# Kernel optimization log

Hardware: AMD Instinct MI355X
Metric: run time of the kernel (lower is better)

The kernel has to match this reference:

```python
import jax, jax.numpy as jnp
import numpy as np

H = 256   # hidden_size
IN = 2    # adding-problem input features
B, T = 128, 1024


def setup_inputs() -> dict:
    key = jax.random.key(0)
    ks = jax.random.split(key, 12)
    sc = 1.0 / np.sqrt(H)
    u = lambda k, shape: jax.random.uniform(k, shape, minval=-sc, maxval=sc, dtype=jnp.float32)
    return {
        "x": jax.random.normal(ks[0], (B, T, IN), dtype=jnp.float32),
        # GRU weights (torch layout: [3H, in], gate order r, z, n)
        "W_ih": u(ks[1], (3 * H, IN)),
        "W_hh": u(ks[2], (3 * H, H)),
        "b_ih": u(ks[3], (3 * H,)),
        "b_hh": u(ks[4], (3 * H,)),
        # adaptive momentum coefficient beta_t = sigmoid(x W + h U + b)
        "Wb_x": u(ks[5], (IN, 1)),
        "Wb_h": u(ks[6], (H, 1)),
        "b_beta": jnp.zeros((1,), dtype=jnp.float32),
        # momentum step size s (learnable scalar)
        "s": jnp.ones((), dtype=jnp.float32),
        # read-out head Linear(H, 1)
        "W_head": u(ks[7], (1, H)),
        "b_head": u(ks[8], (1,)),
    }


def reference(x, W_ih, W_hh, b_ih, b_hh, Wb_x, Wb_h, b_beta, s, W_head, b_head):
    Bm = x.shape[0]

    def step(carry, x_t):
        h, v = carry                                    # h: [B,H], v: [B,3H]
        beta = jax.nn.sigmoid(x_t @ Wb_x + h @ Wb_h + b_beta)   # [B,1]
        p = x_t @ W_ih.T + b_ih                         # input projection [B,3H]
        v = beta * v + s * p                            # momentum buffer
        gh = h @ W_hh.T + b_hh                          # hidden projection [B,3H]
        vr, vz, vn = jnp.split(v, 3, axis=-1)
        hr, hz, hn = jnp.split(gh, 3, axis=-1)
        r = jax.nn.sigmoid(vr + hr)
        z = jax.nn.sigmoid(vz + hz)
        n = jnp.tanh(vn + r * hn)
        h_new = (1.0 - z) * n + z * h
        return (h_new, v), beta[:, 0]

    h0 = jnp.zeros((Bm, H), dtype=x.dtype)
    v0 = jnp.zeros((Bm, 3 * H), dtype=x.dtype)
    (hT, _), betas = jax.lax.scan(step, (h0, v0), jnp.transpose(x, (1, 0, 2)))
    out = hT @ W_head.T + b_head                        # head on last timestep, [B,1]
    return (out, betas.T)                               # betas: [B,T]
```

## Files before the change

### kernel.cpp

```cpp
#include <hip/hip_runtime.h>

#define HID 256
#define TLEN 1024
#define BATCH 128

typedef _Float16 half2_t __attribute__((ext_vector_type(2)));

__device__ __forceinline__ float fexp2(float x) { return __builtin_amdgcn_exp2f(x); }
__device__ __forceinline__ float frcp(float x)  { return __builtin_amdgcn_rcpf(x); }
__device__ __forceinline__ float fast_sigmoid(float x) {
  return frcp(1.0f + fexp2(-1.442695040888963f * x));
}
__device__ __forceinline__ float fast_tanh(float x) {
  float e = fexp2(2.885390081777927f * x);
  return 1.0f - 2.0f * frcp(e + 1.0f);
}
__device__ __forceinline__ float dot2acc(half2_t a, half2_t b, float c) {
  return __builtin_amdgcn_fdot2(a, b, c, false);
}

#if defined(__has_builtin) && __has_builtin(__builtin_amdgcn_sdot4)
#define SDOT4(a, b, c) __builtin_amdgcn_sdot4((int)(a), (int)(b), (c), false)
#else
__device__ __forceinline__ int SDOT4(int a, int b, int c) {
#pragma unroll
  for (int e = 0; e < 4; ++e)
    c += ((a << (24 - 8 * e)) >> 24) * ((b << (24 - 8 * e)) >> 24);
  return c;
}
#endif

#define DPP_ADD_F(var, ctrl, rmask)                                            \
  var += __builtin_bit_cast(float, __builtin_amdgcn_update_dpp(                \
      0, __builtin_bit_cast(int, var), (ctrl), (rmask), 0xf, true))
#define DPP_PAIR_SUM_I(var)                                                    \
  var += __builtin_amdgcn_update_dpp(0, (var), 0xB1, 0xf, 0xf, true)
#define DPP_MOV_I(dst, src, ctrl)                                              \
  dst = __builtin_amdgcn_update_dpp(0, (src), (ctrl), 0xf, 0xf, true)

__device__ __forceinline__ float wave_sum63(float p) {
  DPP_ADD_F(p, 0x111, 0xf);
  DPP_ADD_F(p, 0x112, 0xf);
  DPP_ADD_F(p, 0x114, 0xf);
  DPP_ADD_F(p, 0x118, 0xf);
  DPP_ADD_F(p, 0x142, 0xa);
  DPP_ADD_F(p, 0x143, 0xc);
  return p;
}

#define LDS_BARRIER() asm volatile("s_waitcnt lgkmcnt(0)\n\ts_barrier" ::: "memory")

__global__ void quant_whh(const float* __restrict__ W_hh, uint4* __restrict__ wq,
                          float* __restrict__ scales) {
  const int r = blockIdx.x * 256 + threadIdx.x;
  if (r >= 768) return;
  const float* row = W_hh + (size_t)r * HID;
  float amax = 0.0f;
  for (int k = 0; k < HID; ++k) amax = fmaxf(amax, fabsf(row[k]));
  amax = fmaxf(amax, 1e-20f);
  scales[r] = amax / 127.0f;
  const float inv = 127.0f / amax;
  const int g = r >> 8, d = r & 255;
  for (int jb = 0; jb < 16; ++jb) {
    unsigned w[4];
#pragma unroll
    for (int u = 0; u < 4; ++u) {
      unsigned bb = 0;
#pragma unroll
      for (int e = 0; e < 4; ++e) {
        int q = (int)rintf(row[jb * 16 + u * 4 + e] * inv);
        bb |= (unsigned)(q & 0xff) << (8 * e);
      }
      w[u] = bb;
    }
    wq[(size_t)(2 * d + (jb & 1)) * 24 + g * 8 + (jb >> 1)] = uint4{w[0], w[1], w[2], w[3]};
  }
}

__global__ __launch_bounds__(512, 1)
void momgru_persistent(const float* __restrict__ x,
                       const float* __restrict__ W_ih,
                       const float* __restrict__ b_ih,
                       const float* __restrict__ b_hh,
                       const float* __restrict__ Wb_x,
                       const float* __restrict__ Wb_h,
                       const float* __restrict__ b_beta,
                       const float* __restrict__ s_ptr,
                       const float* __restrict__ W_head,
                       const float* __restrict__ b_head,
                       const uint4* __restrict__ wq,
                       const float* __restrict__ scales,
                       float* __restrict__ out)
{
  const int b    = blockIdx.x;
  const int tid  = threadIdx.x;
  const int lane = tid & 63;
  const int wv   = tid >> 6;
  const int d    = tid >> 1;
  const int half = tid & 1;

  __shared__ unsigned hbuf[2][HID / 4];
  __shared__ float    red[2][8];
  __shared__ uint4    nlds[4 * 512];

  const uint4* wqt = wq + (size_t)tid * 24;
  uint4 wr[8], wz[8], wn[4];
#pragma unroll
  for (int i = 0; i < 8; ++i) wr[i] = wqt[i];
#pragma unroll
  for (int i = 0; i < 8; ++i) wz[i] = wqt[8 + i];
#pragma unroll
  for (int i = 0; i < 4; ++i) wn[i] = wqt[16 + i];
#pragma unroll
  for (int i = 0; i < 4; ++i) nlds[i * 512 + tid] = wqt[20 + i];

  const half2_t wih_r = half2_t{(_Float16)W_ih[2 * d],             (_Float16)W_ih[2 * d + 1]};
  const half2_t wih_z = half2_t{(_Float16)W_ih[2 * (HID + d)],     (_Float16)W_ih[2 * (HID + d) + 1]};
  const half2_t wih_n = half2_t{(_Float16)W_ih[2 * (2 * HID + d)], (_Float16)W_ih[2 * (2 * HID + d) + 1]};
  const float bih_r = b_ih[d], bih_z = b_ih[HID + d], bih_n = b_ih[2 * HID + d];
  const float bhh_r = b_hh[d], bhh_z = b_hh[HID + d], bhh_n = b_hh[2 * HID + d];
  const float scr = scales[d] * (1.0f / 127.0f);
  const float scz = scales[HID + d] * (1.0f / 127.0f);
  const float scn = scales[2 * HID + d] * (1.0f / 127.0f);
  const half2_t wbx2 = half2_t{(_Float16)Wb_x[0], (_Float16)Wb_x[1]};
  const float bbeta = b_beta[0], sv = s_ptr[0];
  const float wbh_t = Wb_h[d];

  if (tid < HID / 4) { hbuf[0][tid] = 0u; hbuf[1][tid] = 0u; }
  float h_old = 0.0f, vr = 0.0f, vz = 0.0f, vn = 0.0f;
  float hWb = 0.0f;
  float* betas = out + BATCH;
  const float2* xg2 = reinterpret_cast<const float2*>(x + (size_t)b * TLEN * 2);
  float2 xv = xg2[0];
  __syncthreads();

  int cur = 0;
  for (int t = 0; t < TLEN; ++t) {
    const half2_t x2 = half2_t{(_Float16)xv.x, (_Float16)xv.y};
    xv = xg2[(t + 1 < TLEN) ? t + 1 : t];

    const float beta = fast_sigmoid(dot2acc(x2, wbx2, hWb + bbeta));
    vr = beta * vr + sv * dot2acc(x2, wih_r, bih_r);
    vz = beta * vz + sv * dot2acc(x2, wih_z, bih_z);
    vn = beta * vn + sv * dot2acc(x2, wih_n, bih_n);

    int ar = 0, az = 0, an = 0;
    const int4* hb = reinterpret_cast<const int4*>(hbuf[cur]);
#pragma unroll
    for (int i = 0; i < 8; ++i) {
      const int4 hv = hb[2 * i + half];
      const uint4 wnv = (i < 4) ? *(const uint4*)&wn[i] : nlds[(i - 4) * 512 + tid];
      ar = SDOT4(hv.x, wr[i].x, ar);
      az = SDOT4(hv.x, wz[i].x, az);
      an = SDOT4(hv.x, wnv.x, an);
      ar = SDOT4(hv.y, wr[i].y, ar);
      az = SDOT4(hv.y, wz[i].y, az);
      an = SDOT4(hv.y, wnv.y, an);
      ar = SDOT4(hv.z, wr[i].z, ar);
      az = SDOT4(hv.z, wz[i].z, az);
      an = SDOT4(hv.z, wnv.z, an);
      ar = SDOT4(hv.w, wr[i].w, ar);
      az = SDOT4(hv.w, wz[i].w, az);
      an = SDOT4(hv.w, wnv.w, an);
    }
    DPP_PAIR_SUM_I(ar);
    DPP_PAIR_SUM_I(az);
    DPP_PAIR_SUM_I(an);

    const float r = fast_sigmoid(vr + (float)ar * scr + bhh_r);
    const float z = fast_sigmoid(vz + (float)az * scz + bhh_z);
    const float n = fast_tanh(vn + r * ((float)an * scn + bhh_n));
    h_old = (1.0f - z) * n + z * h_old;

    const int nxt = cur ^ 1;
    int q = ((int)rintf(h_old * 127.0f)) & 0xff;
    int q1, q2, q3;
    DPP_MOV_I(q1, q, 0x102);
    DPP_MOV_I(q2, q, 0x104);
    DPP_MOV_I(q3, q, 0x106);
    if ((lane & 7) == 0)
      hbuf[nxt][tid >> 3] = (unsigned)(q | (q1 << 8) | (q2 << 16) | (q3 << 24));

    float p = (half == 0) ? h_old * wbh_t : 0.0f;
    p = wave_sum63(p);
    const int rb = t & 1;
    if (lane == 63) red[rb][wv] = p;
    if (tid == 63) betas[(size_t)b * TLEN + t] = beta;

    LDS_BARRIER();
    hWb = red[rb][0] + red[rb][1] + red[rb][2] + red[rb][3] +
          red[rb][4] + red[rb][5] + red[rb][6] + red[rb][7];
    cur = nxt;
  }

  float hp = (half == 0) ? h_old * W_head[d] : 0.0f;
  hp = wave_sum63(hp);
  if (lane == 63) red[0][wv] = hp;
  __syncthreads();
  if (tid == 0) {
    out[b] = red[0][0] + red[0][1] + red[0][2] + red[0][3] +
             red[0][4] + red[0][5] + red[0][6] + red[0][7] + b_head[0];
  }
}

extern "C" void kernel_launch(void* const* d_in, const int* in_sizes, int n_in,
                              void* d_out, int out_size, void* d_ws, size_t ws_size,
                              hipStream_t stream) {
  const float* x      = (const float*)d_in[0];
  const float* W_ih   = (const float*)d_in[1];
  const float* W_hh   = (const float*)d_in[2];
  const float* b_ih   = (const float*)d_in[3];
  const float* b_hh   = (const float*)d_in[4];
  const float* Wb_x   = (const float*)d_in[5];
  const float* Wb_h   = (const float*)d_in[6];
  const float* b_beta = (const float*)d_in[7];
  const float* s      = (const float*)d_in[8];
  const float* W_head = (const float*)d_in[9];
  const float* b_head = (const float*)d_in[10];
  float* out = (float*)d_out;

  uint4* wq      = (uint4*)d_ws;
  float* scales  = (float*)((char*)d_ws + 512 * 24 * 16);

  quant_whh<<<dim3(3), dim3(256), 0, stream>>>(W_hh, wq, scales);
  momgru_persistent<<<dim3(BATCH), dim3(512), 0, stream>>>(
      x, W_ih, b_ih, b_hh, Wb_x, Wb_h, b_beta, s, W_head, b_head,
      (const uint4*)wq, (const float*)scales, out);
}
```

Before: 983.6 us.

## Map each 4-thread group to two hidden units so all int8 weights fit in registers

Changes the work split from two threads per hidden unit to four threads per pair of hidden units, each thread covering a quarter of the K dimension for six gate rows. The weight layout from the quantization kernel is changed to match, so all 24 uint4 weight chunks per thread stay in VGPRs and the LDS spill buffer for the n-gate weights goes away. Each h load is reused across six rows instead of three. The cost is an extra DPP reduction stage, duplicated per-unit gate math, and higher register pressure.

New measurement: 1.097 ms. 1.11x slower.

```diff
diff --git a/kernel.cpp b/kernel.cpp
--- a/kernel.cpp
+++ b/kernel.cpp
@@ -33,8 +33,8 @@
 #define DPP_ADD_F(var, ctrl, rmask)                                            \
   var += __builtin_bit_cast(float, __builtin_amdgcn_update_dpp(                \
       0, __builtin_bit_cast(int, var), (ctrl), (rmask), 0xf, true))
-#define DPP_PAIR_SUM_I(var)                                                    \
-  var += __builtin_amdgcn_update_dpp(0, (var), 0xB1, 0xf, 0xf, true)
+#define DPP_ADD_I(var, ctrl)                                                   \
+  var += __builtin_amdgcn_update_dpp(0, (var), (ctrl), 0xf, 0xf, true)
 #define DPP_MOV_I(dst, src, ctrl)                                              \
   dst = __builtin_amdgcn_update_dpp(0, (src), (ctrl), 0xf, 0xf, true)
 
@@ -60,20 +60,23 @@
   amax = fmaxf(amax, 1e-20f);
   scales[r] = amax / 127.0f;
   const float inv = 127.0f / amax;
-  const int g = r >> 8, d = r & 255;
-  for (int jb = 0; jb < 16; ++jb) {
+  const int g = r >> 8, dd = r & 255;
+  const int dgrp = dd >> 1, e = dd & 1;
+  for (int c = 0; c < 16; ++c) {
     unsigned w[4];
 #pragma unroll
     for (int u = 0; u < 4; ++u) {
       unsigned bb = 0;
 #pragma unroll
-      for (int e = 0; e < 4; ++e) {
-        int q = (int)rintf(row[jb * 16 + u * 4 + e] * inv);
-        bb |= (unsigned)(q & 0xff) << (8 * e);
+      for (int ee = 0; ee < 4; ++ee) {
+        int qv = (int)rintf(row[c * 16 + u * 4 + ee] * inv);
+        bb |= (unsigned)(qv & 0xff) << (8 * ee);
       }
       w[u] = bb;
     }
-    wq[(size_t)(2 * d + (jb & 1)) * 24 + g * 8 + (jb >> 1)] = uint4{w[0], w[1], w[2], w[3]};
+    const int i = c >> 2, q = c & 3;
+    wq[(size_t)(4 * dgrp + q) * 24 + (g * 2 + e) * 4 + i] =
+        uint4{w[0], w[1], w[2], w[3]};
   }
 }
 
@@ -96,38 +99,41 @@
   const int tid  = threadIdx.x;
   const int lane = tid & 63;
   const int wv   = tid >> 6;
-  const int d    = tid >> 1;
-  const int half = tid & 1;
+  const int dgrp = tid >> 2;
+  const int q    = tid & 3;
+  const int d0   = 2 * dgrp, d1 = d0 + 1;
 
   __shared__ unsigned hbuf[2][HID / 4];
   __shared__ float    red[2][8];
-  __shared__ uint4    nlds[4 * 512];
 
   const uint4* wqt = wq + (size_t)tid * 24;
-  uint4 wr[8], wz[8], wn[4];
-#pragma unroll
-  for (int i = 0; i < 8; ++i) wr[i] = wqt[i];
-#pragma unroll
-  for (int i = 0; i < 8; ++i) wz[i] = wqt[8 + i];
-#pragma unroll
-  for (int i = 0; i < 4; ++i) wn[i] = wqt[16 + i];
-#pragma unroll
-  for (int i = 0; i < 4; ++i) nlds[i * 512 + tid] = wqt[20 + i];
-
-  const half2_t wih_r = half2_t{(_Float16)W_ih[2 * d],             (_Float16)W_ih[2 * d + 1]};
-  const half2_t wih_z = half2_t{(_Float16)W_ih[2 * (HID + d)],     (_Float16)W_ih[2 * (HID + d) + 1]};
-  const half2_t wih_n = half2_t{(_Float16)W_ih[2 * (2 * HID + d)], (_Float16)W_ih[2 * (2 * HID + d) + 1]};
-  const float bih_r = b_ih[d], bih_z = b_ih[HID + d], bih_n = b_ih[2 * HID + d];
-  const float bhh_r = b_hh[d], bhh_z = b_hh[HID + d], bhh_n = b_hh[2 * HID + d];
-  const float scr = scales[d] * (1.0f / 127.0f);
-  const float scz = scales[HID + d] * (1.0f / 127.0f);
-  const float scn = scales[2 * HID + d] * (1.0f / 127.0f);
+  uint4 w[24];
+#pragma unroll
+  for (int i = 0; i < 24; ++i) w[i] = wqt[i];
+
+  const half2_t wih_r0 = half2_t{(_Float16)W_ih[2 * d0],             (_Float16)W_ih[2 * d0 + 1]};
+  const half2_t wih_r1 = half2_t{(_Float16)W_ih[2 * d1],             (_Float16)W_ih[2 * d1 + 1]};
+  const half2_t wih_z0 = half2_t{(_Float16)W_ih[2 * (HID + d0)],     (_Float16)W_ih[2 * (HID + d0) + 1]};
+  const half2_t wih_z1 = half2_t{(_Float16)W_ih[2 * (HID + d1)],     (_Float16)W_ih[2 * (HID + d1) + 1]};
+  const half2_t wih_n0 = half2_t{(_Float16)W_ih[2 * (2 * HID + d0)], (_Float16)W_ih[2 * (2 * HID + d0) + 1]};
+  const half2_t wih_n1 = half2_t{(_Float16)W_ih[2 * (2 * HID + d1)], (_Float16)W_ih[2 * (2 * HID + d1) + 1]};
+  const float bih_r0 = b_ih[d0], bih_r1 = b_ih[d1];
+  const float bih_z0 = b_ih[HID + d0], bih_z1 = b_ih[HID + d1];
+  const float bih_n0 = b_ih[2 * HID + d0], bih_n1 = b_ih[2 * HID + d1];
+  const float bhh_r0 = b_hh[d0], bhh_r1 = b_hh[d1];
+  const float bhh_z0 = b_hh[HID + d0], bhh_z1 = b_hh[HID + d1];
+  const float bhh_n0 = b_hh[2 * HID + d0], bhh_n1 = b_hh[2 * HID + d1];
+  const float sc_r0 = scales[d0] * (1.0f / 127.0f), sc_r1 = scales[d1] * (1.0f / 127.0f);
+  const float sc_z0 = scales[HID + d0] * (1.0f / 127.0f), sc_z1 = scales[HID + d1] * (1.0f / 127.0f);
+  const float sc_n0 = scales[2 * HID + d0] * (1.0f / 127.0f), sc_n1 = scales[2 * HID + d1] * (1.0f / 127.0f);
   const half2_t wbx2 = half2_t{(_Float16)Wb_x[0], (_Float16)Wb_x[1]};
   const float bbeta = b_beta[0], sv = s_ptr[0];
-  const float wbh_t = Wb_h[d];
-
-  if (tid < HID / 4) { hbuf[0][tid] = 0u; hbuf[1][tid] = 0u; }
-  float h_old = 0.0f, vr = 0.0f, vz = 0.0f, vn = 0.0f;
+  const float wbh0 = Wb_h[d0], wbh1 = Wb_h[d1];
+  const float wh0 = W_head[d0], wh1 = W_head[d1];
+
+  if (tid < 128) reinterpret_cast<unsigned*>(hbuf)[tid] = 0u;
+  float h0 = 0.0f, h1 = 0.0f;
+  float vr0 = 0.0f, vr1 = 0.0f, vz0 = 0.0f, vz1 = 0.0f, vn0 = 0.0f, vn1 = 0.0f;
   float hWb = 0.0f;
   float* betas = out + BATCH;
   const float2* xg2 = reinterpret_cast<const float2*>(x + (size_t)b * TLEN * 2);
@@ -140,48 +146,51 @@
     xv = xg2[(t + 1 < TLEN) ? t + 1 : t];
 
     const float beta = fast_sigmoid(dot2acc(x2, wbx2, hWb + bbeta));
-    vr = beta * vr + sv * dot2acc(x2, wih_r, bih_r);
-    vz = beta * vz + sv * dot2acc(x2, wih_z, bih_z);
-    vn = beta * vn + sv * dot2acc(x2, wih_n, bih_n);
-
-    int ar = 0, az = 0, an = 0;
+    vr0 = beta * vr0 + sv * dot2acc(x2, wih_r0, bih_r0);
+    vr1 = beta * vr1 + sv * dot2acc(x2, wih_r1, bih_r1);
+    vz0 = beta * vz0 + sv * dot2acc(x2, wih_z0, bih_z0);
+    vz1 = beta * vz1 + sv * dot2acc(x2, wih_z1, bih_z1);
+    vn0 = beta * vn0 + sv * dot2acc(x2, wih_n0, bih_n0);
+    vn1 = beta * vn1 + sv * dot2acc(x2, wih_n1, bih_n1);
+
+    int acc[6] = {0, 0, 0, 0, 0, 0};
     const int4* hb = reinterpret_cast<const int4*>(hbuf[cur]);
 #pragma unroll
-    for (int i = 0; i < 8; ++i) {
-      const int4 hv = hb[2 * i + half];
-      const uint4 wnv = (i < 4) ? *(const uint4*)&wn[i] : nlds[(i - 4) * 512 + tid];
-      ar = SDOT4(hv.x, wr[i].x, ar);
-      az = SDOT4(hv.x, wz[i].x, az);
-      an = SDOT4(hv.x, wnv.x, an);
-      ar = SDOT4(hv.y, wr[i].y, ar);
-      az = SDOT4(hv.y, wz[i].y, az);
-      an = SDOT4(hv.y, wnv.y, an);
-      ar = SDOT4(hv.z, wr[i].z, ar);
-      az = SDOT4(hv.z, wz[i].z, az);
-      an = SDOT4(hv.z, wnv.z, an);
-      ar = SDOT4(hv.w, wr[i].w, ar);
-      az = SDOT4(hv.w, wz[i].w, az);
-      an = SDOT4(hv.w, wnv.w, an);
+    for (int i = 0; i < 4; ++i) {
+      const int4 hv = hb[4 * i + q];
+#pragma unroll
+      for (int rl = 0; rl < 6; ++rl) {
+        const uint4 ww = w[rl * 4 + i];
+        acc[rl] = SDOT4(hv.x, ww.x, acc[rl]);
+        acc[rl] = SDOT4(hv.y, ww.y, acc[rl]);
+        acc[rl] = SDOT4(hv.z, ww.z, acc[rl]);
+        acc[rl] = SDOT4(hv.w, ww.w, acc[rl]);
+      }
     }
-    DPP_PAIR_SUM_I(ar);
-    DPP_PAIR_SUM_I(az);
-    DPP_PAIR_SUM_I(an);
-
-    const float r = fast_sigmoid(vr + (float)ar * scr + bhh_r);
-    const float z = fast_sigmoid(vz + (float)az * scz + bhh_z);
-    const float n = fast_tanh(vn + r * ((float)an * scn + bhh_n));
-    h_old = (1.0f - z) * n + z * h_old;
+#pragma unroll
+    for (int rl = 0; rl < 6; ++rl) {
+      DPP_ADD_I(acc[rl], 0xB1);
+      DPP_ADD_I(acc[rl], 0x4E);
+    }
+
+    const float r0 = fast_sigmoid(vr0 + (float)acc[0] * sc_r0 + bhh_r0);
+    const float r1 = fast_sigmoid(vr1 + (float)acc[1] * sc_r1 + bhh_r1);
+    const float z0 = fast_sigmoid(vz0 + (float)acc[2] * sc_z0 + bhh_z0);
+    const float z1 = fast_sigmoid(vz1 + (float)acc[3] * sc_z1 + bhh_z1);
+    const float n0 = fast_tanh(vn0 + r0 * ((float)acc[4] * sc_n0 + bhh_n0));
+    const float n1 = fast_tanh(vn1 + r1 * ((float)acc[5] * sc_n1 + bhh_n1));
+    h0 = (1.0f - z0) * n0 + z0 * h0;
+    h1 = (1.0f - z1) * n1 + z1 * h1;
 
     const int nxt = cur ^ 1;
-    int q = ((int)rintf(h_old * 127.0f)) & 0xff;
-    int q1, q2, q3;
-    DPP_MOV_I(q1, q, 0x102);
-    DPP_MOV_I(q2, q, 0x104);
-    DPP_MOV_I(q3, q, 0x106);
-    if ((lane & 7) == 0)
-      hbuf[nxt][tid >> 3] = (unsigned)(q | (q1 << 8) | (q2 << 16) | (q3 << 24));
-
-    float p = (half == 0) ? h_old * wbh_t : 0.0f;
+    const int qb0 = ((int)rintf(h0 * 127.0f)) & 0xff;
+    const int qb1 = ((int)rintf(h1 * 127.0f)) & 0xff;
+    const int q16 = qb0 | (qb1 << 8);
+    int qhi;
+    DPP_MOV_I(qhi, q16, 0x104);
+    if ((tid & 7) == 0) hbuf[nxt][tid >> 3] = (unsigned)(q16 | (qhi << 16));
+
+    float p = (q == 0) ? h0 * wbh0 + h1 * wbh1 : 0.0f;
     p = wave_sum63(p);
     const int rb = t & 1;
     if (lane == 63) red[rb][wv] = p;
@@ -193,7 +202,7 @@
     cur = nxt;
   }
 
-  float hp = (half == 0) ? h_old * W_head[d] : 0.0f;
+  float hp = (q == 0) ? h0 * wh0 + h1 * wh1 : 0.0f;
   hp = wave_sum63(hp);
   if (lane == 63) red[0][wv] = hp;
   __syncthreads();
@@ -219,8 +228,8 @@
   const float* b_head = (const float*)d_in[10];
   float* out = (float*)d_out;
 
-  uint4* wq      = (uint4*)d_ws;
-  float* scales  = (float*)((char*)d_ws + 512 * 24 * 16);
+  uint4* wq     = (uint4*)d_ws;
+  float* scales = (float*)((char*)d_ws + 512 * 24 * 16);
 
   quant_whh<<<dim3(3), dim3(256), 0, stream>>>(W_hh, wq, scales);
   momgru_persistent<<<dim3(BATCH), dim3(512), 0, stream>>>(
```

## Keep all int8 W_hh in registers and reorder step to overlap matvec with beta

Applied to the files above, without the earlier changes.

Keeps the entire n-gate int8 weight slice in registers instead of splitting half into LDS, and changes the K layout so each thread reads a contiguous half of h. The step is reordered so the int8 matvec runs before the beta reduction read, letting the cross-wave hWb sum be consumed later in the step. The scalar s is folded into W_ih and b_ih at setup, and the custom lgkmcnt+s_barrier is replaced by __syncthreads. Keeping more weights in registers raises register pressure and risks spills.

Result: faster. 960.9 us (-2.3%).

```diff
diff --git a/kernel.cpp b/kernel.cpp
--- a/kernel.cpp
+++ b/kernel.cpp
@@ -33,8 +33,8 @@
 #define DPP_ADD_F(var, ctrl, rmask)                                            \
   var += __builtin_bit_cast(float, __builtin_amdgcn_update_dpp(                \
       0, __builtin_bit_cast(int, var), (ctrl), (rmask), 0xf, true))
-#define DPP_PAIR_SUM_I(var)                                                    \
-  var += __builtin_amdgcn_update_dpp(0, (var), 0xB1, 0xf, 0xf, true)
+#define DPP_ADD_I(var, ctrl)                                                   \
+  var += __builtin_amdgcn_update_dpp(0, (var), (ctrl), 0xf, 0xf, true)
 #define DPP_MOV_I(dst, src, ctrl)                                              \
   dst = __builtin_amdgcn_update_dpp(0, (src), (ctrl), 0xf, 0xf, true)
 
@@ -47,8 +47,6 @@
   DPP_ADD_F(p, 0x143, 0xc);
   return p;
 }
-
-#define LDS_BARRIER() asm volatile("s_waitcnt lgkmcnt(0)\n\ts_barrier" ::: "memory")
 
 __global__ void quant_whh(const float* __restrict__ W_hh, uint4* __restrict__ wq,
                           float* __restrict__ scales) {
@@ -61,19 +59,21 @@
   scales[r] = amax / 127.0f;
   const float inv = 127.0f / amax;
   const int g = r >> 8, d = r & 255;
-  for (int jb = 0; jb < 16; ++jb) {
-    unsigned w[4];
-#pragma unroll
-    for (int u = 0; u < 4; ++u) {
-      unsigned bb = 0;
-#pragma unroll
-      for (int e = 0; e < 4; ++e) {
-        int q = (int)rintf(row[jb * 16 + u * 4 + e] * inv);
-        bb |= (unsigned)(q & 0xff) << (8 * e);
+  for (int half = 0; half < 2; ++half) {
+    for (int j = 0; j < 8; ++j) {
+      unsigned w[4];
+#pragma unroll
+      for (int u = 0; u < 4; ++u) {
+        unsigned bb = 0;
+#pragma unroll
+        for (int e = 0; e < 4; ++e) {
+          int qv = (int)rintf(row[128 * half + 16 * j + 4 * u + e] * inv);
+          bb |= (unsigned)(qv & 0xff) << (8 * e);
+        }
+        w[u] = bb;
       }
-      w[u] = bb;
+      wq[(size_t)(2 * d + half) * 24 + g * 8 + j] = uint4{w[0], w[1], w[2], w[3]};
     }
-    wq[(size_t)(2 * d + (jb & 1)) * 24 + g * 8 + (jb >> 1)] = uint4{w[0], w[1], w[2], w[3]};
   }
 }
 
@@ -99,36 +99,34 @@
   const int d    = tid >> 1;
   const int half = tid & 1;
 
-  __shared__ unsigned hbuf[2][HID / 4];
+  __shared__ unsigned hq[2][64];
   __shared__ float    red[2][8];
-  __shared__ uint4    nlds[4 * 512];
 
   const uint4* wqt = wq + (size_t)tid * 24;
-  uint4 wr[8], wz[8], wn[4];
-#pragma unroll
-  for (int i = 0; i < 8; ++i) wr[i] = wqt[i];
-#pragma unroll
-  for (int i = 0; i < 8; ++i) wz[i] = wqt[8 + i];
-#pragma unroll
-  for (int i = 0; i < 4; ++i) wn[i] = wqt[16 + i];
-#pragma unroll
-  for (int i = 0; i < 4; ++i) nlds[i * 512 + tid] = wqt[20 + i];
-
-  const half2_t wih_r = half2_t{(_Float16)W_ih[2 * d],             (_Float16)W_ih[2 * d + 1]};
-  const half2_t wih_z = half2_t{(_Float16)W_ih[2 * (HID + d)],     (_Float16)W_ih[2 * (HID + d) + 1]};
-  const half2_t wih_n = half2_t{(_Float16)W_ih[2 * (2 * HID + d)], (_Float16)W_ih[2 * (2 * HID + d) + 1]};
-  const float bih_r = b_ih[d], bih_z = b_ih[HID + d], bih_n = b_ih[2 * HID + d];
+  uint4 wr[8], wz[8], wn[8];
+#pragma unroll
+  for (int j = 0; j < 8; ++j) wr[j] = wqt[j];
+#pragma unroll
+  for (int j = 0; j < 8; ++j) wz[j] = wqt[8 + j];
+#pragma unroll
+  for (int j = 0; j < 8; ++j) wn[j] = wqt[16 + j];
+
+  const float sv = s_ptr[0];
+  const half2_t wih_r = half2_t{(_Float16)(sv * W_ih[2 * d]),             (_Float16)(sv * W_ih[2 * d + 1])};
+  const half2_t wih_z = half2_t{(_Float16)(sv * W_ih[2 * (HID + d)]),     (_Float16)(sv * W_ih[2 * (HID + d) + 1])};
+  const half2_t wih_n = half2_t{(_Float16)(sv * W_ih[2 * (2 * HID + d)]), (_Float16)(sv * W_ih[2 * (2 * HID + d) + 1])};
+  const float bih_r = sv * b_ih[d], bih_z = sv * b_ih[HID + d], bih_n = sv * b_ih[2 * HID + d];
   const float bhh_r = b_hh[d], bhh_z = b_hh[HID + d], bhh_n = b_hh[2 * HID + d];
-  const float scr = scales[d] * (1.0f / 127.0f);
-  const float scz = scales[HID + d] * (1.0f / 127.0f);
-  const float scn = scales[2 * HID + d] * (1.0f / 127.0f);
+  const float sc_r = scales[d] * (1.0f / 127.0f);
+  const float sc_z = scales[HID + d] * (1.0f / 127.0f);
+  const float sc_n = scales[2 * HID + d] * (1.0f / 127.0f);
   const half2_t wbx2 = half2_t{(_Float16)Wb_x[0], (_Float16)Wb_x[1]};
-  const float bbeta = b_beta[0], sv = s_ptr[0];
+  const float bbeta = b_beta[0];
   const float wbh_t = Wb_h[d];
 
-  if (tid < HID / 4) { hbuf[0][tid] = 0u; hbuf[1][tid] = 0u; }
+  if (tid < 128) reinterpret_cast<unsigned*>(hq)[tid] = 0u;
+  if (tid < 16) reinterpret_cast<float*>(red)[tid] = 0.0f;
   float h_old = 0.0f, vr = 0.0f, vz = 0.0f, vn = 0.0f;
-  float hWb = 0.0f;
   float* betas = out + BATCH;
   const float2* xg2 = reinterpret_cast<const float2*>(x + (size_t)b * TLEN * 2);
   float2 xv = xg2[0];
@@ -136,60 +134,58 @@
 
   int cur = 0;
   for (int t = 0; t < TLEN; ++t) {
+    int ar = 0, az = 0, an = 0;
+    const int4* hb = reinterpret_cast<const int4*>(hq[cur]);
+#pragma unroll
+    for (int j = 0; j < 8; ++j) {
+      const int4 hv = hb[8 * half + j];
+      ar = SDOT4(hv.x, wr[j].x, ar);
+      az = SDOT4(hv.x, wz[j].x, az);
+      an = SDOT4(hv.x, wn[j].x, an);
+      ar = SDOT4(hv.y, wr[j].y, ar);
+      az = SDOT4(hv.y, wz[j].y, az);
+      an = SDOT4(hv.y, wn[j].y, an);
+      ar = SDOT4(hv.z, wr[j].z, ar);
+      az = SDOT4(hv.z, wz[j].z, az);
+      an = SDOT4(hv.z, wn[j].z, an);
+      ar = SDOT4(hv.w, wr[j].w, ar);
+      az = SDOT4(hv.w, wz[j].w, az);
+      an = SDOT4(hv.w, wn[j].w, an);
+    }
+    DPP_ADD_I(ar, 0xB1);
+    DPP_ADD_I(az, 0xB1);
+    DPP_ADD_I(an, 0xB1);
+
+    const int rp = (t + 1) & 1;
+    const float hWb = red[rp][0] + red[rp][1] + red[rp][2] + red[rp][3] +
+                      red[rp][4] + red[rp][5] + red[rp][6] + red[rp][7];
     const half2_t x2 = half2_t{(_Float16)xv.x, (_Float16)xv.y};
     xv = xg2[(t + 1 < TLEN) ? t + 1 : t];
-
     const float beta = fast_sigmoid(dot2acc(x2, wbx2, hWb + bbeta));
-    vr = beta * vr + sv * dot2acc(x2, wih_r, bih_r);
-    vz = beta * vz + sv * dot2acc(x2, wih_z, bih_z);
-    vn = beta * vn + sv * dot2acc(x2, wih_n, bih_n);
-
-    int ar = 0, az = 0, an = 0;
-    const int4* hb = reinterpret_cast<const int4*>(hbuf[cur]);
-#pragma unroll
-    for (int i = 0; i < 8; ++i) {
-      const int4 hv = hb[2 * i + half];
-      const uint4 wnv = (i < 4) ? *(const uint4*)&wn[i] : nlds[(i - 4) * 512 + tid];
-      ar = SDOT4(hv.x, wr[i].x, ar);
-      az = SDOT4(hv.x, wz[i].x, az);
-      an = SDOT4(hv.x, wnv.x, an);
-      ar = SDOT4(hv.y, wr[i].y, ar);
-      az = SDOT4(hv.y, wz[i].y, az);
-      an = SDOT4(hv.y, wnv.y, an);
-      ar = SDOT4(hv.z, wr[i].z, ar);
-      az = SDOT4(hv.z, wz[i].z, az);
-      an = SDOT4(hv.z, wnv.z, an);
-      ar = SDOT4(hv.w, wr[i].w, ar);
-      az = SDOT4(hv.w, wz[i].w, az);
-      an = SDOT4(hv.w, wnv.w, an);
-    }
-    DPP_PAIR_SUM_I(ar);
-    DPP_PAIR_SUM_I(az);
-    DPP_PAIR_SUM_I(an);
-
-    const float r = fast_sigmoid(vr + (float)ar * scr + bhh_r);
-    const float z = fast_sigmoid(vz + (float)az * scz + bhh_z);
-    const float n = fast_tanh(vn + r * ((float)an * scn + bhh_n));
+    vr = beta * vr + dot2acc(x2, wih_r, bih_r);
+    vz = beta * vz + dot2acc(x2, wih_z, bih_z);
+    vn = beta * vn + dot2acc(x2, wih_n, bih_n);
+
+    const float r = fast_sigmoid(vr + (float)ar * sc_r + bhh_r);
+    const float z = fast_sigmoid(vz + (float)az * sc_z + bhh_z);
+    const float n = fast_tanh(vn + r * ((float)an * sc_n + bhh_n));
     h_old = (1.0f - z) * n + z * h_old;
 
     const int nxt = cur ^ 1;
-    int q = ((int)rintf(h_old * 127.0f)) & 0xff;
-    int q1, q2, q3;
-    DPP_MOV_I(q1, q, 0x102);
-    DPP_MOV_I(q2, q, 0x104);
-    DPP_MOV_I(q3, q, 0x106);
-    if ((lane & 7) == 0)
-      hbuf[nxt][tid >> 3] = (unsigned)(q | (q1 << 8) | (q2 << 16) | (q3 << 24));
+    const int qb = ((int)rintf(h_old * 127.0f)) & 0xff;
+    int q2, q4, q6;
+    DPP_MOV_I(q2, qb, 0x102);
+    DPP_MOV_I(q4, qb, 0x104);
+    DPP_MOV_I(q6, qb, 0x106);
+    if ((tid & 7) == 0)
+      hq[nxt][tid >> 3] = (unsigned)(qb | (q2 << 8) | (q4 << 16) | (q6 << 24));
 
     float p = (half == 0) ? h_old * wbh_t : 0.0f;
     p = wave_sum63(p);
-    const int rb = t & 1;
-    if (lane == 63) red[rb][wv] = p;
+    if (lane == 63) red[t & 1][wv] = p;
     if (tid == 63) betas[(size_t)b * TLEN + t] = beta;
 
-    LDS_BARRIER();
-    hWb = red[rb][0] + red[rb][1] + red[rb][2] + red[rb][3] +
-          red[rb][4] + red[rb][5] + red[rb][6] + red[rb][7];
+    __syncthreads();
     cur = nxt;
   }
 
@@ -219,8 +215,8 @@
   const float* b_head = (const float*)d_in[10];
   float* out = (float*)d_out;
 
-  uint4* wq      = (uint4*)d_ws;
-  float* scales  = (float*)((char*)d_ws + 512 * 24 * 16);
+  uint4* wq     = (uint4*)d_ws;
+  float* scales = (float*)((char*)d_ws + 512 * 24 * 16);
 
   quant_whh<<<dim3(3), dim3(256), 0, stream>>>(W_hh, wq, scales);
   momgru_persistent<<<dim3(BATCH), dim3(512), 0, stream>>>(
```
